# Performance work log

Measured on AMD Instinct MI355X. Metric: run time of the kernel, lower is better.

Reference implementation:

```python
import jax, jax.numpy as jnp
import numpy as np

EPS = 1e-5


def _knn_group(q, p, kk):
    """q: [3,Nq] query points, p: [3,M] reference points. Returns
    features [4,Nq,kk] = (residual xyz, distance) and neighbors [3,Nq,kk]."""
    qt, pt = q.T, p.T  # [Nq,3], [M,3]
    d2 = (jnp.sum(qt * qt, axis=1)[:, None]
          + jnp.sum(pt * pt, axis=1)[None, :]
          - 2.0 * qt @ pt.T)                       # [Nq,M] squared dists
    _, idx = jax.lax.top_k(-d2, kk)                 # kk nearest -> [Nq,kk]
    nn = pt[idx]                                    # [Nq,kk,3]
    resi = nn - qt[:, None, :]
    dist = jnp.linalg.norm(resi, axis=-1, keepdims=True)
    feat = jnp.concatenate([resi, dist], axis=-1)   # [Nq,kk,4]
    return feat.transpose(2, 0, 1), nn.transpose(2, 0, 1)


def _group_norm(x, groups, w, b):
    B, C, N, K = x.shape
    xg = x.reshape(B, groups, C // groups, N, K)
    mu = xg.mean(axis=(2, 3, 4), keepdims=True)
    var = xg.var(axis=(2, 3, 4), keepdims=True)
    xg = (xg - mu) * jax.lax.rsqrt(var + EPS)
    return xg.reshape(B, C, N, K) * w[None, :, None, None] + b[None, :, None, None]


def _forward(points0, points1, w1, b1, gn1_w, gn1_b, w2, b2, gn2_w, gn2_b,
             k, wt_np, perm_np):
    B, _, N = points0.shape
    feats, grouped = [], []
    for i in range(B):  # per-sample loop: split sizes are data-dependent (as in original)
        N0 = int(N * wt_np[i, 0]); N1 = N - N0
        k0 = int(k * wt_np[i, 0]); k1 = k - k0
        newp = jnp.concatenate([points0[i][:, perm_np[i, 0, :N0]],
                                points1[i][:, perm_np[i, 1, :N1]]], axis=-1)  # [3,N]
        f0, g0 = _knn_group(newp, points0[i], k0)
        f1, g1 = _knn_group(newp, points1[i], k1)
        feats.append(jnp.concatenate([f0, f1], axis=-1))
        grouped.append(jnp.concatenate([g0, g1], axis=-1))
    x = jnp.stack(feats)        # [B,4,N,k]
    gp = jnp.stack(grouped)     # [B,3,N,k]
    # 1x1 conv -> GroupNorm -> ReLU, twice
    x = jnp.einsum('bcnk,oc->bonk', x, w1) + b1[None, :, None, None]
    x = jax.nn.relu(_group_norm(x, w1.shape[0] // 8, gn1_w, gn1_b))
    x = jnp.einsum('bcnk,oc->bonk', x, w2) + b2[None, :, None, None]
    x = jax.nn.relu(_group_norm(x, w2.shape[0] // 8, gn2_w, gn2_b))
    scores = jnp.max(x, axis=1)                 # [B,N,k]
    wts = jax.nn.softmax(scores, axis=-1)       # softmax over neighbors
    return jnp.sum(wts[:, None, :, :] * gp, axis=-1)  # [B,3,N]


def setup_inputs() -> dict:
    key = jax.random.key(0)
    B, N, K = 8, 4096, 32
    C1, C2 = 32, 64
    ks = jax.random.split(key, 8)
    points0 = jax.random.normal(ks[0], (B, 3, N), jnp.float32)
    points1 = jax.random.normal(ks[1], (B, 3, N), jnp.float32)
    weighted_t = jax.random.uniform(ks[2], (B, 2), jnp.float32, 0.25, 0.75)
    perm = jax.vmap(lambda kk: jax.random.permutation(kk, N))(
        jax.random.split(ks[3], B * 2)).reshape(B, 2, N).astype(jnp.int32)
    w1 = 0.1 * jax.random.normal(ks[4], (C1, 4), jnp.float32)
    b1 = jnp.zeros((C1,), jnp.float32)
    gn1_w = jnp.ones((C1,), jnp.float32)
    gn1_b = jnp.zeros((C1,), jnp.float32)
    w2 = 0.1 * jax.random.normal(ks[5], (C2, C1), jnp.float32)
    b2 = jnp.zeros((C2,), jnp.float32)
    gn2_w = jnp.ones((C2,), jnp.float32)
    gn2_b = jnp.zeros((C2,), jnp.float32)
    return dict(points0=points0, points1=points1, k=K, weighted_t=weighted_t,
                perm=perm, w1=w1, b1=b1, gn1_w=gn1_w, gn1_b=gn1_b,
                w2=w2, b2=b2, gn2_w=gn2_w, gn2_b=gn2_b)


def reference(points0, points1, k, weighted_t, perm, w1, b1, gn1_w, gn1_b,
              w2, b2, gn2_w, gn2_b):
    wt_np = np.asarray(weighted_t)   # concrete: drives static split sizes
    perm_np = np.asarray(perm)
    return _forward(points0, points1, w1, b1, gn1_w, gn1_b, w2, b2,
                    gn2_w, gn2_b, int(k), wt_np, perm_np)
```

## Files before the change

kernel.cpp:

```cpp
#include <hip/hip_runtime.h>
#include <math.h>

#define RQ 6
constexpr int PBINS = 12;

typedef __attribute__((ext_vector_type(8))) short s8v;
typedef __attribute__((ext_vector_type(4))) float f32x4;

__device__ inline unsigned short f2bf(float x) {
    const unsigned int u = __float_as_uint(x);
    return (unsigned short)((u + 0x7FFFu + ((u >> 16) & 1u)) >> 16);
}

__constant__ float ZB[63] = {
    -2.1539f, -1.8627f, -1.6759f, -1.5341f, -1.4178f, -1.3180f, -1.2299f, -1.1503f,
    -1.0775f, -1.0100f, -0.9468f, -0.8871f, -0.8305f, -0.7764f, -0.7245f, -0.6745f,
    -0.6261f, -0.5791f, -0.5334f, -0.4888f, -0.4451f, -0.4023f, -0.3601f, -0.3186f,
    -0.2776f, -0.2372f, -0.1971f, -0.1573f, -0.1178f, -0.0784f, -0.0392f,  0.0000f,
     0.0392f,  0.0784f,  0.1178f,  0.1573f,  0.1971f,  0.2372f,  0.2776f,  0.3186f,
     0.3601f,  0.4023f,  0.4451f,  0.4888f,  0.5334f,  0.5791f,  0.6261f,  0.6745f,
     0.7245f,  0.7764f,  0.8305f,  0.8871f,  0.9468f,  1.0100f,  1.0775f,  1.1503f,
     1.2299f,  1.3180f,  1.4178f,  1.5341f,  1.6759f,  1.8627f,  2.1539f };

__global__ __launch_bounds__(1024) void zbin_kernel(
    const float* __restrict__ p0, const float* __restrict__ p1,
    float4* __restrict__ sp, int* __restrict__ starts, int N)
{
    __shared__ int cnt[64], off[64], cur[64];
    const int t = threadIdx.x;
    const int bl = blockIdx.x;
    const int b = bl >> 1, list = bl & 1;
    const float* rb = (list ? p1 : p0) + (size_t)(b * 3) * N;
    if (t < 64) { cnt[t] = 0; cur[t] = 0; }
    __syncthreads();
    int mybin[4]; float mx[4], my[4], mz[4];
    for (int i = 0; i < 4; ++i) {
        const int idx = i * 1024 + t;
        const float z = rb[2 * N + idx];
        mx[i] = rb[idx]; my[i] = rb[N + idx]; mz[i] = z;
        int bin = 0;
#pragma unroll
        for (int s = 32; s; s >>= 1)
            if (bin + s <= 63 && z >= ZB[bin + s - 1]) bin += s;
        mybin[i] = bin;
        atomicAdd(&cnt[bin], 1);
    }
    __syncthreads();
    if (t < 64) {
        const int v = cnt[t];
        int x = v;
#pragma unroll
        for (int o = 1; o < 64; o <<= 1) {
            const int y = __shfl_up(x, o);
            if (t >= o) x += y;
        }
        off[t] = x - v;
        starts[bl * 65 + t] = x - v;
        if (t == 63) starts[bl * 65 + 64] = x;
    }
    __syncthreads();
    for (int i = 0; i < 4; ++i) {
        const int bin = mybin[i];
        const int pos = off[bin] + atomicAdd(&cur[bin], 1);
        sp[(size_t)bl * 4096 + pos] =
            make_float4(mx[i], my[i], mz[i],
                        fmaf(mx[i], mx[i], fmaf(my[i], my[i], mz[i] * mz[i])));
    }
}


__device__ __forceinline__ void mstep(const float4 pc, int pos, int end,
                                      float qx, float qy, float qz, float qq,
                                      unsigned& mn)
{
    const float dt = fmaf(qz, pc.z, fmaf(qy, pc.y, qx * pc.x));
    const float d = fmaxf(fmaf(-2.f, dt, pc.w + qq), 0.f);
    const unsigned key = (pos < end) ? __float_as_uint(d) : 0xFFFFFFFFu;
    mn = min(mn, key);
}

__device__ __forceinline__ void cstep(const float4 pc, int pos, int end,
                                      float qx, float qy, float qz, float qq,
                                      unsigned Tu,
                                      unsigned* __restrict__ ck,
                                      unsigned* __restrict__ cp,
                                      int& cnt)
{
    const float dt = fmaf(qz, pc.z, fmaf(qy, pc.y, qx * pc.x));
    const float d = fmaxf(fmaf(-2.f, dt, pc.w + qq), 0.f);
    const unsigned key = __float_as_uint(d);
    const bool pred = (pos < end) && (key <= Tu);
    const unsigned long long bal = __ballot(pred);
    const unsigned below = __builtin_amdgcn_mbcnt_hi(
        (unsigned)(bal >> 32), __builtin_amdgcn_mbcnt_lo((unsigned)bal, 0u));
    const unsigned idx = (unsigned)cnt + below;
    if (pred && idx < 64u) { ck[idx] = key; cp[idx] = (unsigned)pos; }
    cnt += (int)__popcll(bal);
}

__device__ __forceinline__ void cscan(const float4* __restrict__ L,
                                      int bs, int be,
                                      float qx, float qy, float qz, float qq,
                                      unsigned Tu,
                                      unsigned* __restrict__ ck,
                                      unsigned* __restrict__ cp,
                                      int& cnt, int lane)
{
    for (int p = bs; p < be; p += 64) {
        const int pos = p + lane;
        const float4 pc = L[min(pos, be - 1)];
        cstep(pc, pos, be, qx, qy, qz, qq, Tu, ck, cp, cnt);
    }
}

__device__ __forceinline__ void sort_write(
    const unsigned* __restrict__ ck, const unsigned* __restrict__ cp, int cnt,
    const float4* __restrict__ L, int kk, int obase,
    float qx, float qy, float qz, float4* __restrict__ feat, int lane)
{
    unsigned vk = (lane < cnt) ? ck[lane] : 0xFFFFFFFFu;
    unsigned vp = (lane < cnt) ? cp[lane] : 0xFFFFFFFFu;
#pragma unroll
    for (int k2 = 2; k2 <= 64; k2 <<= 1) {
#pragma unroll
        for (int jj = k2 >> 1; jj; jj >>= 1) {
            const unsigned yk = __shfl_xor(vk, jj);
            const unsigned yp = __shfl_xor(vp, jj);
            const bool keepmin = (((lane & jj) == 0) == ((lane & k2) == 0));
            const bool lt = (vk < yk) || ((vk == yk) && (vp < yp));
            const bool sely = keepmin ? (!lt) : lt;
            vk = sely ? yk : vk;
            vp = sely ? yp : vp;
        }
    }
    if (lane < kk) {
        const float4 pc = L[vp & 4095u];
        const float rx = pc.x - qx, ry = pc.y - qy, rz = pc.z - qz;
        feat[obase + lane] =
            make_float4(rx, ry, rz, sqrtf(fmaf(rx, rx, fmaf(ry, ry, rz * rz))));
    }
}

__device__ __forceinline__ void qpush(unsigned (&kh)[RQ], unsigned (&kl)[RQ],
                                      unsigned key, unsigned pos)
{
    bool cb[RQ];
#pragma unroll
    for (int s = 0; s < RQ; ++s) cb[s] = key < kh[s];
#pragma unroll
    for (int s = RQ - 1; s >= 1; --s) {
        kh[s] = cb[s - 1] ? kh[s - 1] : (cb[s] ? key : kh[s]);
        kl[s] = cb[s - 1] ? kl[s - 1] : (cb[s] ? pos : kl[s]);
    }
    kh[0] = cb[0] ? key : kh[0];
    kl[0] = cb[0] ? pos : kl[0];
}

__device__ __forceinline__ void pop_extract(
    unsigned (&kh)[RQ], unsigned (&kl)[RQ], int kk,
    const float4* __restrict__ L, int obase,
    float qx, float qy, float qz, float4* __restrict__ feat, int lane)
{
    unsigned mwin = 0;
    for (int rr = 0; rr < kk; ++rr) {
        unsigned gg = kh[0];
#pragma unroll
        for (int off = 32; off; off >>= 1) gg = min(gg, __shfl_xor(gg, off));
        const bool tied = (kh[0] == gg);
        unsigned mc;
        const unsigned long long bal = __ballot(tied);
        if (bal & (bal - 1)) {
            mc = tied ? kl[0] : 0xFFFFFFFFu;
#pragma unroll
            for (int off = 32; off; off >>= 1) mc = min(mc, __shfl_xor(mc, off));
        } else {
            mc = __shfl(kl[0], (int)__ffsll((long long)bal) - 1);
        }
        const bool w = tied && (kl[0] == mc);
        if (lane == rr) mwin = mc;
#pragma unroll
        for (int s = 0; s < RQ - 1; ++s) {
            kh[s] = w ? kh[s + 1] : kh[s];
            kl[s] = w ? kl[s + 1] : kl[s];
        }
        kh[RQ - 1] = w ? 0xFFFFFFFFu : kh[RQ - 1];
        kl[RQ - 1] = w ? 0xFFFFFFFFu : kl[RQ - 1];
    }
    if (lane < kk) {
        const float4 pc = L[mwin & 4095u];
        const float rx = pc.x - qx, ry = pc.y - qy, rz = pc.z - qz;
        feat[obase + lane] =
            make_float4(rx, ry, rz, sqrtf(fmaf(rx, rx, fmaf(ry, ry, rz * rz))));
    }
}

__device__ __forceinline__ void fallback_full(
    const float4* __restrict__ L, int Npts, int kk, int obase,
    float qx, float qy, float qz, float qq,
    float4* __restrict__ feat, int lane)
{
    unsigned kh[RQ], kl[RQ];
#pragma unroll
    for (int s = 0; s < RQ; ++s) { kh[s] = 0xFFFFFFFFu; kl[s] = 0xFFFFFFFFu; }
    for (int p = 0; p < Npts; p += 64) {
        const int pos = p + lane;
        const float4 pc = L[min(pos, Npts - 1)];
        const float dt = fmaf(qz, pc.z, fmaf(qy, pc.y, qx * pc.x));
        const float d = fmaxf(fmaf(-2.f, dt, pc.w + qq), 0.f);
        const unsigned key = (pos < Npts) ? __float_as_uint(d) : 0xFFFFFFFFu;
        qpush(kh, kl, key, (unsigned)pos);
    }
    pop_extract(kh, kl, kk, L, obase, qx, qy, qz, feat, lane);
}

__global__ __launch_bounds__(256) void knn_kernel(
    const float* __restrict__ p0, const float* __restrict__ p1,
    const float* __restrict__ wt, const int* __restrict__ perm,
    const float4* __restrict__ sp, const int* __restrict__ starts,
    float4* __restrict__ feat, float4* __restrict__ newp, int N)
{
    __shared__ unsigned ck0s[256], cp0s[256], ck1s[256], cp1s[256];
    const int lane = threadIdx.x & 63;
    const int wv = threadIdx.x >> 6;
    const int gwave = (int)((blockIdx.x * 256 + threadIdx.x) >> 6);
    const int b = gwave / N;
    const int n = gwave - b * N;
    const int q = b * N + n;

    unsigned* __restrict__ ck0 = ck0s + wv * 64;
    unsigned* __restrict__ cp0 = cp0s + wv * 64;
    unsigned* __restrict__ ck1 = ck1s + wv * 64;
    unsigned* __restrict__ cp1 = cp1s + wv * 64;

    const float wt0 = wt[b * 2];
    const int N0 = (int)(N * wt0);
    const int k0 = (int)(32 * wt0);
    const int kk0 = k0, kk1 = 32 - k0;

    int j; const float* src;
    if (n < N0) { j = perm[(b * 2) * N + n];            src = p0; }
    else        { j = perm[(b * 2 + 1) * N + (n - N0)]; src = p1; }
    const float qx = __uint_as_float(__builtin_amdgcn_readfirstlane(
                         __float_as_uint(src[(b * 3) * N + j])));
    const float qy = __uint_as_float(__builtin_amdgcn_readfirstlane(
                         __float_as_uint(src[(b * 3 + 1) * N + j])));
    const float qz = __uint_as_float(__builtin_amdgcn_readfirstlane(
                         __float_as_uint(src[(b * 3 + 2) * N + j])));
    const float qq = qx * qx + qy * qy + qz * qz;

    const float bv = (lane < 63) ? ZB[lane] : 3.0e38f;
    const int qbin = __popcll(__ballot(qz >= bv));
    int lo = qbin - PBINS / 2;
    lo = lo < 0 ? 0 : (lo > 64 - PBINS ? 64 - PBINS : lo);
    const int hi = lo + PBINS;

    if (lane == 0) newp[q] = make_float4(qx, qy, qz, 0.f);

    const int bl0 = b * 2, bl1 = b * 2 + 1;
    const float4* L0 = sp + (size_t)bl0 * 4096;
    const float4* L1 = sp + (size_t)bl1 * 4096;
    const int s00 = starts[bl0 * 65 + lo], e00 = starts[bl0 * 65 + hi];
    const int s01 = starts[bl1 * 65 + lo], e01 = starts[bl1 * 65 + hi];

    const int nch0 = (e00 - s00 + 63) >> 6;
    const int nch1 = (e01 - s01 + 63) >> 6;
    const int ncm = nch0 < nch1 ? nch0 : nch1;

    unsigned mn0 = 0xFFFFFFFFu, mn1 = 0xFFFFFFFFu;
    {
        float4 c0v = make_float4(0.f, 0.f, 0.f, 0.f);
        float4 c1v = make_float4(0.f, 0.f, 0.f, 0.f);
        if (nch0 > 0) c0v = L0[min(s00 + lane, e00 - 1)];
        if (nch1 > 0) c1v = L1[min(s01 + lane, e01 - 1)];
        for (int ch = 0; ch < ncm; ++ch) {
            const int pf0 = min(ch + 1, nch0 - 1), pf1 = min(ch + 1, nch1 - 1);
            const float4 n0v = L0[min(s00 + (pf0 << 6) + lane, e00 - 1)];
            const float4 n1v = L1[min(s01 + (pf1 << 6) + lane, e01 - 1)];
            mstep(c0v, s00 + (ch << 6) + lane, e00, qx, qy, qz, qq, mn0);
            mstep(c1v, s01 + (ch << 6) + lane, e01, qx, qy, qz, qq, mn1);
            c0v = n0v; c1v = n1v;
        }
        for (int ch = ncm; ch < nch0; ++ch) {
            const float4 n0v = L0[min(s00 + (min(ch + 1, nch0 - 1) << 6) + lane, e00 - 1)];
            mstep(c0v, s00 + (ch << 6) + lane, e00, qx, qy, qz, qq, mn0);
            c0v = n0v;
        }
        for (int ch = ncm; ch < nch1; ++ch) {
            const float4 n1v = L1[min(s01 + (min(ch + 1, nch1 - 1) << 6) + lane, e01 - 1)];
            mstep(c1v, s01 + (ch << 6) + lane, e01, qx, qy, qz, qq, mn1);
            c1v = n1v;
        }
    }

    unsigned x0 = mn0, x1 = mn1;
#pragma unroll
    for (int k2 = 2; k2 <= 64; k2 <<= 1) {
#pragma unroll
        for (int jj = k2 >> 1; jj; jj >>= 1) {
            const unsigned y0 = __shfl_xor(x0, jj);
            const unsigned y1 = __shfl_xor(x1, jj);
            const bool keepmin = (((lane & jj) == 0) == ((lane & k2) == 0));
            x0 = keepmin ? min(x0, y0) : (x0 > y0 ? x0 : y0);
            x1 = keepmin ? min(x1, y1) : (x1 > y1 ? x1 : y1);
        }
    }
    const unsigned Tu0 = (unsigned)__shfl((int)x0, kk0 - 1);
    const unsigned Tu1 = (unsigned)__shfl((int)x1, kk1 - 1);
    const float T0f = __uint_as_float(Tu0);
    const float T1f = __uint_as_float(Tu1);

    int cnt0 = 0, cnt1 = 0;
    {
        float4 c0v = make_float4(0.f, 0.f, 0.f, 0.f);
        float4 c1v = make_float4(0.f, 0.f, 0.f, 0.f);
        if (nch0 > 0) c0v = L0[min(s00 + lane, e00 - 1)];
        if (nch1 > 0) c1v = L1[min(s01 + lane, e01 - 1)];
        for (int ch = 0; ch < ncm; ++ch) {
            const int pf0 = min(ch + 1, nch0 - 1), pf1 = min(ch + 1, nch1 - 1);
            const float4 n0v = L0[min(s00 + (pf0 << 6) + lane, e00 - 1)];
            const float4 n1v = L1[min(s01 + (pf1 << 6) + lane, e01 - 1)];
            cstep(c0v, s00 + (ch << 6) + lane, e00, qx, qy, qz, qq, Tu0, ck0, cp0, cnt0);
            cstep(c1v, s01 + (ch << 6) + lane, e01, qx, qy, qz, qq, Tu1, ck1, cp1, cnt1);
            c0v = n0v; c1v = n1v;
        }
        for (int ch = ncm; ch < nch0; ++ch) {
            const float4 n0v = L0[min(s00 + (min(ch + 1, nch0 - 1) << 6) + lane, e00 - 1)];
            cstep(c0v, s00 + (ch << 6) + lane, e00, qx, qy, qz, qq, Tu0, ck0, cp0, cnt0);
            c0v = n0v;
        }
        for (int ch = ncm; ch < nch1; ++ch) {
            const float4 n1v = L1[min(s01 + (min(ch + 1, nch1 - 1) << 6) + lane, e01 - 1)];
            cstep(c1v, s01 + (ch << 6) + lane, e01, qx, qy, qz, qq, Tu1, ck1, cp1, cnt1);
            c1v = n1v;
        }
    }

    {
        for (int br = hi; br <= 63; ++br) {
            const float dz = ZB[br - 1] - qz;
            if (dz * dz * 0.99999f > T0f) break;
            cscan(L0, starts[bl0 * 65 + br], starts[bl0 * 65 + br + 1],
                  qx, qy, qz, qq, Tu0, ck0, cp0, cnt0, lane);
        }
        for (int blft = lo - 1; blft >= 0; --blft) {
            const float dz = qz - ZB[blft];
            if (dz * dz * 0.99999f > T0f) break;
            cscan(L0, starts[bl0 * 65 + blft], starts[bl0 * 65 + blft + 1],
                  qx, qy, qz, qq, Tu0, ck0, cp0, cnt0, lane);
        }
        for (int br = hi; br <= 63; ++br) {
            const float dz = ZB[br - 1] - qz;
            if (dz * dz * 0.99999f > T1f) break;
            cscan(L1, starts[bl1 * 65 + br], starts[bl1 * 65 + br + 1],
                  qx, qy, qz, qq, Tu1, ck1, cp1, cnt1, lane);
        }
        for (int blft = lo - 1; blft >= 0; --blft) {
            const float dz = qz - ZB[blft];
            if (dz * dz * 0.99999f > T1f) break;
            cscan(L1, starts[bl1 * 65 + blft], starts[bl1 * 65 + blft + 1],
                  qx, qy, qz, qq, Tu1, ck1, cp1, cnt1, lane);
        }
    }

    const int ob0 = (q << 5), ob1 = (q << 5) + k0;
    if (cnt0 <= 64)
        sort_write(ck0, cp0, cnt0, L0, kk0, ob0, qx, qy, qz, feat, lane);
    else
        fallback_full(L0, N, kk0, ob0, qx, qy, qz, qq, feat, lane);
    if (cnt1 <= 64)
        sort_write(ck1, cp1, cnt1, L1, kk1, ob1, qx, qy, qz, feat, lane);
    else
        fallback_full(L1, N, kk1, ob1, qx, qy, qz, qq, feat, lane);
}

__global__ __launch_bounds__(256) void moment_stats_kernel(
    const float4* __restrict__ feat, float* __restrict__ stats1, int N)
{
    const int t = threadIdx.x, lane = t & 63;
    const int bpb = 64;
    const int b = blockIdx.x / bpb;
    const int ppb = (N * 32) / bpb;
    const size_t base = (size_t)b * N * 32 + (size_t)(blockIdx.x % bpb) * ppb;
    float a[14];
#pragma unroll
    for (int i = 0; i < 14; ++i) a[i] = 0.f;
    for (int i = t; i < ppb; i += 256) {
        const float4 f = feat[base + i];
        a[0] += f.x; a[1] += f.y; a[2] += f.z; a[3] += f.w;
        a[4] = fmaf(f.x, f.x, a[4]);  a[5] = fmaf(f.x, f.y, a[5]);
        a[6] = fmaf(f.x, f.z, a[6]);  a[7] = fmaf(f.x, f.w, a[7]);
        a[8] = fmaf(f.y, f.y, a[8]);  a[9] = fmaf(f.y, f.z, a[9]);
        a[10] = fmaf(f.y, f.w, a[10]); a[11] = fmaf(f.z, f.z, a[11]);
        a[12] = fmaf(f.z, f.w, a[12]); a[13] = fmaf(f.w, f.w, a[13]);
    }
#pragma unroll
    for (int i = 0; i < 14; ++i) {
        float x = a[i];
#pragma unroll
        for (int o = 32; o; o >>= 1) x += __shfl_down(x, o);
        a[i] = x;
    }
    __shared__ float sm[14];
    if (t < 14) sm[t] = 0.f;
    __syncthreads();
    if (lane == 0) {
#pragma unroll
        for (int i = 0; i < 14; ++i) atomicAdd(&sm[i], a[i]);
    }
    __syncthreads();
    if (t < 14) atomicAdd(&stats1[b * 14 + t], sm[t]);
}

template <int MODE>
__global__ __launch_bounds__(256) void conv2_pass_kernel(
    const float4* __restrict__ feat,
    const float* __restrict__ w1, const float* __restrict__ b1,
    const float* __restrict__ gn1w, const float* __restrict__ gn1b,
    const float* __restrict__ stats1,
    const float* __restrict__ w2, const float* __restrict__ b2,
    const float* __restrict__ gn2w, const float* __restrict__ gn2b,
    float* __restrict__ stats2,
    const float4* __restrict__ newp, float* __restrict__ out,
    int N, float inv_cnt)
{
    const int t = threadIdx.x, lane = t & 63, wv = t >> 6;
    const int quad = lane >> 4, col = lane & 15;
    const int bpb = (N * 32) / 512;
    const int b = blockIdx.x / bpb;
    const int pblock = (blockIdx.x - b * bpb) * 512;
    const size_t pbase = (size_t)b * N * 32 + pblock + wv * 128;

    __shared__ float sfin[24];
    __shared__ float sacc[16];
    __shared__ unsigned short h_lds[512 * 40];
    __shared__ float ssc[512];

    if (t < 16) sacc[t] = 0.f;
    if (t < 4) {
        const float cnt = (float)(N * 32);
        const float* mm = stats1 + b * 14;
        const float S0 = mm[0], S1 = mm[1], S2 = mm[2], S3 = mm[3];
        float sum = 0.f, sq = 0.f;
        for (int cch = 0; cch < 8; ++cch) {
            const int cid = t * 8 + cch;
            const float4 w = ((const float4*)w1)[cid];
            const float bb = b1[cid];
            const float ws = w.x * S0 + w.y * S1 + w.z * S2 + w.w * S3;
            const float wMw =
                w.x * w.x * mm[4] + w.y * w.y * mm[8] + w.z * w.z * mm[11] +
                w.w * w.w * mm[13] +
                2.f * (w.x * w.y * mm[5] + w.x * w.z * mm[6] + w.x * w.w * mm[7] +
                       w.y * w.z * mm[9] + w.y * w.w * mm[10] + w.z * w.w * mm[12]);
            sum += cnt * bb + ws;
            sq += cnt * bb * bb + 2.f * bb * ws + wMw;
        }
        const float mu = sum * inv_cnt, var = sq * inv_cnt - mu * mu;
        sfin[2 * t] = mu; sfin[2 * t + 1] = rsqrtf(var + 1e-5f);
    }
    if (MODE == 1 && t >= 4 && t < 12) {
        const int g = t - 4;
        const float S = stats2[b * 16 + g], Q = stats2[b * 16 + 8 + g];
        const float mu = S * inv_cnt, var = Q * inv_cnt - mu * mu;
        sfin[8 + 2 * g] = mu; sfin[8 + 2 * g + 1] = rsqrtf(var + 1e-5f);
    }
    __syncthreads();

    const int c1 = lane & 31, pt = lane >> 5;
    const float4 w1r = ((const float4*)w1)[c1];
    const float b1c = b1[c1];
    const int g1 = c1 >> 3;
    const float sc1 = sfin[2 * g1 + 1] * gn1w[c1];
    const float sh1 = gn1b[c1] - sfin[2 * g1] * sc1;

    for (int it = 0; it < 64; ++it) {
        const size_t p = pbase + it * 2;
        const float4 f = feat[p + pt];
        const float y = b1c + w1r.x * f.x + w1r.y * f.y + w1r.z * f.z + w1r.w * f.w;
        const float h = fmaxf(0.f, fmaf(y, sc1, sh1));
        h_lds[(wv * 128 + it * 2 + pt) * 40 + c1] = f2bf(h);
    }

    s8v afr[4];
#pragma unroll
    for (int T = 0; T < 4; ++T) {
        const int row = T * 16 + col;
#pragma unroll
        for (int j2 = 0; j2 < 8; ++j2)
            afr[T][j2] = (short)f2bf(w2[row * 32 + quad * 8 + j2]);
    }

    float b2v[4][4], sc2v[4][4], sh2v[4][4];
#pragma unroll
    for (int T = 0; T < 4; ++T)
#pragma unroll
        for (int r4 = 0; r4 < 4; ++r4) {
            const int cch = T * 16 + quad * 4 + r4;
            b2v[T][r4] = b2[cch];
            if (MODE == 1) {
                const int g2 = cch >> 3;
                const float sc = sfin[8 + 2 * g2 + 1] * gn2w[cch];
                sc2v[T][r4] = sc;
                sh2v[T][r4] = gn2b[cch] - sfin[8 + 2 * g2] * sc + b2[cch] * sc;
            }
        }

    float gsum[4] = {0, 0, 0, 0}, gsq[4] = {0, 0, 0, 0};

    for (int pt16 = 0; pt16 < 8; ++pt16) {
        const int row = wv * 128 + pt16 * 16 + col;
        const s8v bfr = *(const s8v*)&h_lds[row * 40 + quad * 8];
        f32x4 acc[4];
#pragma unroll
        for (int T = 0; T < 4; ++T) {
            acc[T] = (f32x4){0.f, 0.f, 0.f, 0.f};
            acc[T] = __builtin_amdgcn_mfma_f32_16x16x32_bf16(afr[T], bfr, acc[T], 0, 0, 0);
        }
        if (MODE == 0) {
#pragma unroll
            for (int T = 0; T < 4; ++T)
#pragma unroll
                for (int r4 = 0; r4 < 4; ++r4) {
                    const float v = acc[T][r4] + b2v[T][r4];
                    gsum[T] += v;
                    gsq[T] = fmaf(v, v, gsq[T]);
                }
        } else {
            float s = -3.0e38f;
#pragma unroll
            for (int T = 0; T < 4; ++T)
#pragma unroll
                for (int r4 = 0; r4 < 4; ++r4)
                    s = fmaxf(s, fmaxf(0.f, fmaf(acc[T][r4], sc2v[T][r4], sh2v[T][r4])));
            s = fmaxf(s, __shfl_xor(s, 16));
            s = fmaxf(s, __shfl_xor(s, 32));
            if (quad == 0) ssc[wv * 128 + pt16 * 16 + col] = s;
        }
    }

    if (MODE == 0) {
#pragma unroll
        for (int T = 0; T < 4; ++T) {
#pragma unroll
            for (int o = 1; o < 16; o <<= 1) {
                gsum[T] += __shfl_xor(gsum[T], o);
                gsq[T] += __shfl_xor(gsq[T], o);
            }
            gsum[T] += __shfl_xor(gsum[T], 16);
            gsq[T] += __shfl_xor(gsq[T], 16);
        }
        if (lane == 0) {
#pragma unroll
            for (int T = 0; T < 4; ++T) {
                atomicAdd(&sacc[2 * T], gsum[T]);
                atomicAdd(&sacc[8 + 2 * T], gsq[T]);
            }
        }
        if (lane == 32) {
#pragma unroll
            for (int T = 0; T < 4; ++T) {
                atomicAdd(&sacc[2 * T + 1], gsum[T]);
                atomicAdd(&sacc[8 + 2 * T + 1], gsq[T]);
            }
        }
        __syncthreads();
        if (t < 16) atomicAdd(&stats2[b * 16 + t], sacc[t]);
    } else {
        __syncthreads();
        const int qi = t >> 4, sub = t & 15;
        const int qg = (b * N * 32 + pblock) / 32 + qi;
        const int n = qg - b * N;
        const float s0 = ssc[qi * 32 + sub], s1 = ssc[qi * 32 + 16 + sub];
        float mx = fmaxf(s0, s1);
#pragma unroll
        for (int o = 8; o; o >>= 1) mx = fmaxf(mx, __shfl_xor(mx, o));
        const float e0 = __expf(s0 - mx), e1 = __expf(s1 - mx);
        float ssum = e0 + e1;
#pragma unroll
        for (int o = 8; o; o >>= 1) ssum += __shfl_xor(ssum, o);
        const float4 qc = newp[qg];
        const float4 f0 = feat[(size_t)qg * 32 + sub];
        const float4 f1 = feat[(size_t)qg * 32 + 16 + sub];
        float ax = e0 * (qc.x + f0.x) + e1 * (qc.x + f1.x);
        float ay = e0 * (qc.y + f0.y) + e1 * (qc.y + f1.y);
        float az = e0 * (qc.z + f0.z) + e1 * (qc.z + f1.z);
#pragma unroll
        for (int o = 8; o; o >>= 1) {
            ax += __shfl_xor(ax, o);
            ay += __shfl_xor(ay, o);
            az += __shfl_xor(az, o);
        }
        if (sub == 0) {
            const float inv = 1.f / ssum;
            out[(b * 3 + 0) * N + n] = ax * inv;
            out[(b * 3 + 1) * N + n] = ay * inv;
            out[(b * 3 + 2) * N + n] = az * inv;
        }
    }
}

extern "C" void kernel_launch(void* const* d_in, const int* in_sizes, int n_in,
                              void* d_out, int out_size, void* d_ws, size_t ws_size,
                              hipStream_t stream)
{
    const float* p0   = (const float*)d_in[0];
    const float* p1   = (const float*)d_in[1];
    const float* wt   = (const float*)d_in[3];
    const int*   perm = (const int*)d_in[4];
    const float* w1   = (const float*)d_in[5];
    const float* b1   = (const float*)d_in[6];
    const float* gn1w = (const float*)d_in[7];
    const float* gn1b = (const float*)d_in[8];
    const float* w2   = (const float*)d_in[9];
    const float* b2   = (const float*)d_in[10];
    const float* gn2w = (const float*)d_in[11];
    const float* gn2b = (const float*)d_in[12];
    float* out = (float*)d_out;

    const int B = in_sizes[3] / 2;
    const int N = in_sizes[0] / (3 * B);

    char* ws = (char*)d_ws;
    float4* spts = (float4*)ws;
    size_t off = (size_t)B * 2 * 4096 * sizeof(float4);
    float4* feat = (float4*)(ws + off);       off += (size_t)B * N * 32 * sizeof(float4);
    float4* newp = (float4*)(ws + off);       off += (size_t)B * N * sizeof(float4);
    float* stats1 = (float*)(ws + off);       off += (size_t)B * 14 * sizeof(float);
    float* stats2 = (float*)(ws + off);       off += (size_t)B * 16 * sizeof(float);
    int* starts = (int*)(ws + off);

    hipMemsetAsync(stats1, 0, (size_t)B * 30 * sizeof(float), stream);

    const float inv_cnt = 1.f / (8.f * (float)N * 32.f);

    zbin_kernel<<<B * 2, 1024, 0, stream>>>(p0, p1, spts, starts, N);

    knn_kernel<<<(B * N) / 4, 256, 0, stream>>>(
        p0, p1, wt, perm, spts, starts, feat, newp, N);

    moment_stats_kernel<<<B * 64, 256, 0, stream>>>(feat, stats1, N);

    conv2_pass_kernel<0><<<(B * N * 32) / 512, 256, 0, stream>>>(
        feat, w1, b1, gn1w, gn1b, stats1, w2, b2, gn2w, gn2b, stats2,
        newp, out, N, inv_cnt);

    conv2_pass_kernel<1><<<(B * N * 32) / 512, 256, 0, stream>>>(
        feat, w1, b1, gn1w, gn1b, stats1, w2, b2, gn2w, gn2b, stats2,
        newp, out, N, inv_cnt);
}
```

Before: 354.9 us.

## Use fixed rank window for KNN candidate scan and cache distances in registers

```diff
diff --git a/kernel.cpp b/kernel.cpp
--- a/kernel.cpp
+++ b/kernel.cpp
@@ -2,7 +2,8 @@
 #include <math.h>
 
 #define RQ 6
-constexpr int PBINS = 12;
+constexpr int WRANKS = 768;
+constexpr int WCH = 12;
 
 typedef __attribute__((ext_vector_type(8))) short s8v;
 typedef __attribute__((ext_vector_type(4))) float f32x4;
@@ -69,32 +70,18 @@
 }
 
 
-__device__ __forceinline__ void mstep(const float4 pc, int pos, int end,
-                                      float qx, float qy, float qz, float qq,
-                                      unsigned& mn)
-{
-    const float dt = fmaf(qz, pc.z, fmaf(qy, pc.y, qx * pc.x));
-    const float d = fmaxf(fmaf(-2.f, dt, pc.w + qq), 0.f);
-    const unsigned key = (pos < end) ? __float_as_uint(d) : 0xFFFFFFFFu;
-    mn = min(mn, key);
-}
-
-__device__ __forceinline__ void cstep(const float4 pc, int pos, int end,
-                                      float qx, float qy, float qz, float qq,
-                                      unsigned Tu,
+__device__ __forceinline__ void cpush(unsigned key, unsigned pos, unsigned Tu,
+                                      bool valid,
                                       unsigned* __restrict__ ck,
                                       unsigned* __restrict__ cp,
                                       int& cnt)
 {
-    const float dt = fmaf(qz, pc.z, fmaf(qy, pc.y, qx * pc.x));
-    const float d = fmaxf(fmaf(-2.f, dt, pc.w + qq), 0.f);
-    const unsigned key = __float_as_uint(d);
-    const bool pred = (pos < end) && (key <= Tu);
+    const bool pred = valid && (key <= Tu);
     const unsigned long long bal = __ballot(pred);
     const unsigned below = __builtin_amdgcn_mbcnt_hi(
         (unsigned)(bal >> 32), __builtin_amdgcn_mbcnt_lo((unsigned)bal, 0u));
     const unsigned idx = (unsigned)cnt + below;
-    if (pred && idx < 64u) { ck[idx] = key; cp[idx] = (unsigned)pos; }
+    if (pred && idx < 64u) { ck[idx] = key; cp[idx] = pos; }
     cnt += (int)__popcll(bal);
 }
 
@@ -109,7 +96,49 @@
     for (int p = bs; p < be; p += 64) {
         const int pos = p + lane;
         const float4 pc = L[min(pos, be - 1)];
-        cstep(pc, pos, be, qx, qy, qz, qq, Tu, ck, cp, cnt);
+        const float dt = fmaf(qz, pc.z, fmaf(qy, pc.y, qx * pc.x));
+        const float d = fmaxf(fmaf(-2.f, dt, pc.w + qq), 0.f);
+        cpush(__float_as_uint(d), (unsigned)pos, Tu, pos < be, ck, cp, cnt);
+    }
+}
+
+__device__ __forceinline__ void sort2_write(
+    const unsigned* __restrict__ ck0, const unsigned* __restrict__ cp0, int cnt0,
+    const float4* __restrict__ L0, int kk0, int ob0,
+    const unsigned* __restrict__ ck1, const unsigned* __restrict__ cp1, int cnt1,
+    const float4* __restrict__ L1, int kk1, int ob1,
+    float qx, float qy, float qz, float4* __restrict__ feat, int lane)
+{
+    unsigned vk0 = (lane < cnt0) ? ck0[lane] : 0xFFFFFFFFu;
+    unsigned vp0 = (lane < cnt0) ? cp0[lane] : 0xFFFFFFFFu;
+    unsigned vk1 = (lane < cnt1) ? ck1[lane] : 0xFFFFFFFFu;
+    unsigned vp1 = (lane < cnt1) ? cp1[lane] : 0xFFFFFFFFu;
+#pragma unroll
+    for (int k2 = 2; k2 <= 64; k2 <<= 1) {
+#pragma unroll
+        for (int jj = k2 >> 1; jj; jj >>= 1) {
+            const unsigned yk0 = __shfl_xor(vk0, jj), yp0 = __shfl_xor(vp0, jj);
+            const unsigned yk1 = __shfl_xor(vk1, jj), yp1 = __shfl_xor(vp1, jj);
+            const bool keepmin = (((lane & jj) == 0) == ((lane & k2) == 0));
+            const bool lt0 = (vk0 < yk0) || ((vk0 == yk0) && (vp0 < yp0));
+            const bool s0 = keepmin ? (!lt0) : lt0;
+            vk0 = s0 ? yk0 : vk0; vp0 = s0 ? yp0 : vp0;
+            const bool lt1 = (vk1 < yk1) || ((vk1 == yk1) && (vp1 < yp1));
+            const bool s1 = keepmin ? (!lt1) : lt1;
+            vk1 = s1 ? yk1 : vk1; vp1 = s1 ? yp1 : vp1;
+        }
+    }
+    if (lane < kk0) {
+        const float4 pc = L0[vp0 & 4095u];
+        const float rx = pc.x - qx, ry = pc.y - qy, rz = pc.z - qz;
+        feat[ob0 + lane] =
+            make_float4(rx, ry, rz, sqrtf(fmaf(rx, rx, fmaf(ry, ry, rz * rz))));
+    }
+    if (lane < kk1) {
+        const float4 pc = L1[vp1 & 4095u];
+        const float rx = pc.x - qx, ry = pc.y - qy, rz = pc.z - qz;
+        feat[ob1 + lane] =
+            make_float4(rx, ry, rz, sqrtf(fmaf(rx, rx, fmaf(ry, ry, rz * rz))));
     }
 }
 
@@ -213,7 +242,7 @@
     pop_extract(kh, kl, kk, L, obase, qx, qy, qz, feat, lane);
 }
 
-__global__ __launch_bounds__(256) void knn_kernel(
+__global__ __launch_bounds__(256, 4) void knn_kernel(
     const float* __restrict__ p0, const float* __restrict__ p1,
     const float* __restrict__ wt, const int* __restrict__ perm,
     const float4* __restrict__ sp, const int* __restrict__ starts,
@@ -248,47 +277,63 @@
                          __float_as_uint(src[(b * 3 + 2) * N + j])));
     const float qq = qx * qx + qy * qy + qz * qz;
 
+    const int bl0 = b * 2, bl1 = b * 2 + 1;
+    const int stv0 = starts[bl0 * 65 + lane];
+    const int stv1 = starts[bl1 * 65 + lane];
+
     const float bv = (lane < 63) ? ZB[lane] : 3.0e38f;
     const int qbin = __popcll(__ballot(qz >= bv));
-    int lo = qbin - PBINS / 2;
-    lo = lo < 0 ? 0 : (lo > 64 - PBINS ? 64 - PBINS : lo);
-    const int hi = lo + PBINS;
 
     if (lane == 0) newp[q] = make_float4(qx, qy, qz, 0.f);
 
-    const int bl0 = b * 2, bl1 = b * 2 + 1;
     const float4* L0 = sp + (size_t)bl0 * 4096;
     const float4* L1 = sp + (size_t)bl1 * 4096;
-    const int s00 = starts[bl0 * 65 + lo], e00 = starts[bl0 * 65 + hi];
-    const int s01 = starts[bl1 * 65 + lo], e01 = starts[bl1 * 65 + hi];
-
-    const int nch0 = (e00 - s00 + 63) >> 6;
-    const int nch1 = (e01 - s01 + 63) >> 6;
-    const int ncm = nch0 < nch1 ? nch0 : nch1;
-
+
+    const int st0 = __shfl(stv0, qbin);
+    const int en0 = (qbin >= 63) ? N : __shfl(stv0, qbin + 1);
+    const int st1 = __shfl(stv1, qbin);
+    const int en1 = (qbin >= 63) ? N : __shfl(stv1, qbin + 1);
+    int s0 = ((st0 + en0) >> 1) - WRANKS / 2;
+    s0 = s0 < 0 ? 0 : (s0 > N - WRANKS ? N - WRANKS : s0);
+    int s1 = ((st1 + en1) >> 1) - WRANKS / 2;
+    s1 = s1 < 0 ? 0 : (s1 > N - WRANKS ? N - WRANKS : s1);
+    const int e0 = s0 + WRANKS, e1 = s1 + WRANKS;
+
+    const float4* Lb0 = L0 + s0 + lane;
+    const float4* Lb1 = L1 + s1 + lane;
+    unsigned k0v[WCH], k1v[WCH];
     unsigned mn0 = 0xFFFFFFFFu, mn1 = 0xFFFFFFFFu;
     {
-        float4 c0v = make_float4(0.f, 0.f, 0.f, 0.f);
-        float4 c1v = make_float4(0.f, 0.f, 0.f, 0.f);
-        if (nch0 > 0) c0v = L0[min(s00 + lane, e00 - 1)];
-        if (nch1 > 0) c1v = L1[min(s01 + lane, e01 - 1)];
-        for (int ch = 0; ch < ncm; ++ch) {
-            const int pf0 = min(ch + 1, nch0 - 1), pf1 = min(ch + 1, nch1 - 1);
-            const float4 n0v = L0[min(s00 + (pf0 << 6) + lane, e00 - 1)];
-            const float4 n1v = L1[min(s01 + (pf1 << 6) + lane, e01 - 1)];
-            mstep(c0v, s00 + (ch << 6) + lane, e00, qx, qy, qz, qq, mn0);
-            mstep(c1v, s01 + (ch << 6) + lane, e01, qx, qy, qz, qq, mn1);
-            c0v = n0v; c1v = n1v;
-        }
-        for (int ch = ncm; ch < nch0; ++ch) {
-            const float4 n0v = L0[min(s00 + (min(ch + 1, nch0 - 1) << 6) + lane, e00 - 1)];
-            mstep(c0v, s00 + (ch << 6) + lane, e00, qx, qy, qz, qq, mn0);
-            c0v = n0v;
-        }
-        for (int ch = ncm; ch < nch1; ++ch) {
-            const float4 n1v = L1[min(s01 + (min(ch + 1, nch1 - 1) << 6) + lane, e01 - 1)];
-            mstep(c1v, s01 + (ch << 6) + lane, e01, qx, qy, qz, qq, mn1);
-            c1v = n1v;
+        float4 A0[3], A1[3], B0[3], B1[3];
+#pragma unroll
+        for (int c = 0; c < 3; ++c) { A0[c] = Lb0[c << 6]; A1[c] = Lb1[c << 6]; }
+#pragma unroll
+        for (int g = 0; g < 4; ++g) {
+            if (g < 3) {
+#pragma unroll
+                for (int c = 0; c < 3; ++c) {
+                    B0[c] = Lb0[(g * 3 + 3 + c) << 6];
+                    B1[c] = Lb1[(g * 3 + 3 + c) << 6];
+                }
+            }
+#pragma unroll
+            for (int c = 0; c < 3; ++c) {
+                const int ch = g * 3 + c;
+                {
+                    const float dt = fmaf(qz, A0[c].z, fmaf(qy, A0[c].y, qx * A0[c].x));
+                    k0v[ch] = __float_as_uint(fmaxf(fmaf(-2.f, dt, A0[c].w + qq), 0.f));
+                    mn0 = min(mn0, k0v[ch]);
+                }
+                {
+                    const float dt = fmaf(qz, A1[c].z, fmaf(qy, A1[c].y, qx * A1[c].x));
+                    k1v[ch] = __float_as_uint(fmaxf(fmaf(-2.f, dt, A1[c].w + qq), 0.f));
+                    mn1 = min(mn1, k1v[ch]);
+                }
+            }
+            if (g < 3) {
+#pragma unroll
+                for (int c = 0; c < 3; ++c) { A0[c] = B0[c]; A1[c] = B1[c]; }
+            }
         }
     }
 
@@ -310,67 +355,74 @@
     const float T1f = __uint_as_float(Tu1);
 
     int cnt0 = 0, cnt1 = 0;
+#pragma unroll
+    for (int ch = 0; ch < WCH; ++ch) {
+        cpush(k0v[ch], (unsigned)(s0 + (ch << 6) + lane), Tu0, true, ck0, cp0, cnt0);
+        cpush(k1v[ch], (unsigned)(s1 + (ch << 6) + lane), Tu1, true, ck1, cp1, cnt1);
+    }
+
     {
-        float4 c0v = make_float4(0.f, 0.f, 0.f, 0.f);
-        float4 c1v = make_float4(0.f, 0.f, 0.f, 0.f);
-        if (nch0 > 0) c0v = L0[min(s00 + lane, e00 - 1)];
-        if (nch1 > 0) c1v = L1[min(s01 + lane, e01 - 1)];
-        for (int ch = 0; ch < ncm; ++ch) {
-            const int pf0 = min(ch + 1, nch0 - 1), pf1 = min(ch + 1, nch1 - 1);
-            const float4 n0v = L0[min(s00 + (pf0 << 6) + lane, e00 - 1)];
-            const float4 n1v = L1[min(s01 + (pf1 << 6) + lane, e01 - 1)];
-            cstep(c0v, s00 + (ch << 6) + lane, e00, qx, qy, qz, qq, Tu0, ck0, cp0, cnt0);
-            cstep(c1v, s01 + (ch << 6) + lane, e01, qx, qy, qz, qq, Tu1, ck1, cp1, cnt1);
-            c0v = n0v; c1v = n1v;
-        }
-        for (int ch = ncm; ch < nch0; ++ch) {
-            const float4 n0v = L0[min(s00 + (min(ch + 1, nch0 - 1) << 6) + lane, e00 - 1)];
-            cstep(c0v, s00 + (ch << 6) + lane, e00, qx, qy, qz, qq, Tu0, ck0, cp0, cnt0);
-            c0v = n0v;
-        }
-        for (int ch = ncm; ch < nch1; ++ch) {
-            const float4 n1v = L1[min(s01 + (min(ch + 1, nch1 - 1) << 6) + lane, e01 - 1)];
-            cstep(c1v, s01 + (ch << 6) + lane, e01, qx, qy, qz, qq, Tu1, ck1, cp1, cnt1);
-            c1v = n1v;
-        }
-    }
-
-    {
-        for (int br = hi; br <= 63; ++br) {
-            const float dz = ZB[br - 1] - qz;
-            if (dz * dz * 0.99999f > T0f) break;
-            cscan(L0, starts[bl0 * 65 + br], starts[bl0 * 65 + br + 1],
-                  qx, qy, qz, qq, Tu0, ck0, cp0, cnt0, lane);
-        }
-        for (int blft = lo - 1; blft >= 0; --blft) {
-            const float dz = qz - ZB[blft];
-            if (dz * dz * 0.99999f > T0f) break;
-            cscan(L0, starts[bl0 * 65 + blft], starts[bl0 * 65 + blft + 1],
-                  qx, qy, qz, qq, Tu0, ck0, cp0, cnt0, lane);
-        }
-        for (int br = hi; br <= 63; ++br) {
-            const float dz = ZB[br - 1] - qz;
-            if (dz * dz * 0.99999f > T1f) break;
-            cscan(L1, starts[bl1 * 65 + br], starts[bl1 * 65 + br + 1],
-                  qx, qy, qz, qq, Tu1, ck1, cp1, cnt1, lane);
-        }
-        for (int blft = lo - 1; blft >= 0; --blft) {
-            const float dz = qz - ZB[blft];
-            if (dz * dz * 0.99999f > T1f) break;
-            cscan(L1, starts[bl1 * 65 + blft], starts[bl1 * 65 + blft + 1],
-                  qx, qy, qz, qq, Tu1, ck1, cp1, cnt1, lane);
+        const int binL = __popcll(__ballot(stv0 <= s0)) - 1;
+        if (s0 > 0) {
+            const int bs = __shfl(stv0, binL);
+            if (bs < s0) cscan(L0, bs, s0, qx, qy, qz, qq, Tu0, ck0, cp0, cnt0, lane);
+            for (int jb = binL - 1; jb >= 0; --jb) {
+                const float dz = qz - ZB[jb];
+                if (dz * dz * 0.99999f > T0f) break;
+                const int bs2 = __shfl(stv0, jb);
+                const int be2 = __shfl(stv0, jb + 1);
+                cscan(L0, bs2, be2, qx, qy, qz, qq, Tu0, ck0, cp0, cnt0, lane);
+            }
+        }
+        if (e0 < N) {
+            const int binR = __popcll(__ballot(stv0 <= e0)) - 1;
+            const int re = (binR >= 63) ? N : __shfl(stv0, binR + 1);
+            if (e0 < re) cscan(L0, e0, re, qx, qy, qz, qq, Tu0, ck0, cp0, cnt0, lane);
+            for (int jb = binR + 1; jb <= 63; ++jb) {
+                const float dz = ZB[jb - 1] - qz;
+                if (dz * dz * 0.99999f > T0f) break;
+                const int bs2 = __shfl(stv0, jb);
+                const int be2 = (jb >= 63) ? N : __shfl(stv0, jb + 1);
+                cscan(L0, bs2, be2, qx, qy, qz, qq, Tu0, ck0, cp0, cnt0, lane);
+            }
+        }
+        const int binL1 = __popcll(__ballot(stv1 <= s1)) - 1;
+        if (s1 > 0) {
+            const int bs = __shfl(stv1, binL1);
+            if (bs < s1) cscan(L1, bs, s1, qx, qy, qz, qq, Tu1, ck1, cp1, cnt1, lane);
+            for (int jb = binL1 - 1; jb >= 0; --jb) {
+                const float dz = qz - ZB[jb];
+                if (dz * dz * 0.99999f > T1f) break;
+                const int bs2 = __shfl(stv1, jb);
+                const int be2 = __shfl(stv1, jb + 1);
+                cscan(L1, bs2, be2, qx, qy, qz, qq, Tu1, ck1, cp1, cnt1, lane);
+            }
+        }
+        if (e1 < N) {
+            const int binR1 = __popcll(__ballot(stv1 <= e1)) - 1;
+            const int re = (binR1 >= 63) ? N : __shfl(stv1, binR1 + 1);
+            if (e1 < re) cscan(L1, e1, re, qx, qy, qz, qq, Tu1, ck1, cp1, cnt1, lane);
+            for (int jb = binR1 + 1; jb <= 63; ++jb) {
+                const float dz = ZB[jb - 1] - qz;
+                if (dz * dz * 0.99999f > T1f) break;
+                const int bs2 = __shfl(stv1, jb);
+                const int be2 = (jb >= 63) ? N : __shfl(stv1, jb + 1);
+                cscan(L1, bs2, be2, qx, qy, qz, qq, Tu1, ck1, cp1, cnt1, lane);
+            }
         }
     }
 
     const int ob0 = (q << 5), ob1 = (q << 5) + k0;
-    if (cnt0 <= 64)
-        sort_write(ck0, cp0, cnt0, L0, kk0, ob0, qx, qy, qz, feat, lane);
-    else
-        fallback_full(L0, N, kk0, ob0, qx, qy, qz, qq, feat, lane);
-    if (cnt1 <= 64)
-        sort_write(ck1, cp1, cnt1, L1, kk1, ob1, qx, qy, qz, feat, lane);
-    else
-        fallback_full(L1, N, kk1, ob1, qx, qy, qz, qq, feat, lane);
+    if ((cnt0 <= 64) && (cnt1 <= 64)) {
+        sort2_write(ck0, cp0, cnt0, L0, kk0, ob0,
+                    ck1, cp1, cnt1, L1, kk1, ob1,
+                    qx, qy, qz, feat, lane);
+    } else {
+        if (cnt0 <= 64) sort_write(ck0, cp0, cnt0, L0, kk0, ob0, qx, qy, qz, feat, lane);
+        else            fallback_full(L0, N, kk0, ob0, qx, qy, qz, qq, feat, lane);
+        if (cnt1 <= 64) sort_write(ck1, cp1, cnt1, L1, kk1, ob1, qx, qy, qz, feat, lane);
+        else            fallback_full(L1, N, kk1, ob1, qx, qy, qz, qq, feat, lane);
+    }
 }
 
 __global__ __launch_bounds__(256) void moment_stats_kernel(
```

New measurement: 343.0 us. 1.03x faster.
